# Kernel optimization log

Hardware: AMD Instinct MI355X
Metric: run time of the kernel (lower is better)

## Reference

```python
import jax, jax.numpy as jnp
import numpy as np


def _hausdorff(x, y):
    # x, y: [B, C, N, D] point sets per (batch, channel); rows are points.
    x2 = jnp.sum(x * x, axis=-1)                       # [B, C, N]
    y2 = jnp.sum(y * y, axis=-1)                       # [B, C, M]
    xy = jnp.einsum('bcnd,bcmd->bcnm', x, y)           # [B, C, N, M]
    d2 = x2[..., :, None] + y2[..., None, :] - 2.0 * xy
    d = jnp.sqrt(jnp.maximum(d2, 0.0))                 # Euclidean distances
    d_fwd = jnp.max(jnp.min(d, axis=-1), axis=-1)      # max_n min_m, [B, C]
    d_bwd = jnp.max(jnp.min(d, axis=-2), axis=-1)      # max_m min_n, [B, C]
    return jnp.maximum(d_fwd, d_bwd)                   # symmetric Hausdorff [B, C]


def setup_inputs() -> dict:
    key = jax.random.key(0)
    k1, k2 = jax.random.split(key)
    B, C, H, W = 8, 3, 1024, 1024
    inp = jax.random.normal(k1, (B, C, H, W), dtype=jnp.float32)
    tgt = jax.random.normal(k2, (B, C, H, W), dtype=jnp.float32)
    return {'input': inp, 'target': tgt}


def reference(input, target):
    h = _hausdorff(input, target)        # [B, C]
    # original: sum_i mean_c(h[i]) / B == mean over (B, C)
    return jnp.mean(h)
```

## Files before the change

### kernel.cpp

```cpp
#include <hip/hip_runtime.h>
#include <math.h>

constexpr int BC = 24;
constexpr int N  = 1024;
constexpr int D  = 1024;
constexpr int TILE = 128;
constexpr int BK = 32;
constexpr int SK = BK + 8;

typedef short short8 __attribute__((ext_vector_type(8)));
typedef float f32x4  __attribute__((ext_vector_type(4)));

#define FINF 3.402823466e+38f

#define GLDS16(g, l)                                                          \
    __builtin_amdgcn_global_load_lds(                                         \
        (const __attribute__((address_space(1))) void*)(g),                   \
        (__attribute__((address_space(3))) void*)(l), 16, 0, 0)

__device__ inline unsigned pk_bf16(float a, float b) {
    unsigned ua = __float_as_uint(a) + 0x8000u;
    unsigned ub = __float_as_uint(b) + 0x8000u;
    return __builtin_amdgcn_perm(ub, ua, 0x07060302);
}

__global__ __launch_bounds__(256) void prep_kernel(const float* __restrict__ X,
                                                   const float* __restrict__ Y,
                                                   unsigned short* __restrict__ Xbf,
                                                   unsigned short* __restrict__ Ybf,
                                                   float* __restrict__ xn,
                                                   float* __restrict__ yn) {
    int w = threadIdx.x >> 6, lane = threadIdx.x & 63;
    long rid = (long)blockIdx.x * 4 + w;
    bool isY = rid >= (long)BC * N;
    long row = isY ? rid - (long)BC * N : rid;
    const float* src = (isY ? Y : X) + row * D;
    unsigned short* dst = (isY ? Ybf : Xbf) + row * D;
    float s = 0.f;
    #pragma unroll
    for (int q = 0; q < 4; q++) {
        float4 v = ((const float4*)src)[lane + q * 64];
        s += v.x * v.x + v.y * v.y + v.z * v.z + v.w * v.w;
        uint2 p; p.x = pk_bf16(v.x, v.y); p.y = pk_bf16(v.z, v.w);
        ((uint2*)dst)[lane + q * 64] = p;
    }
    #pragma unroll
    for (int m = 1; m < 64; m <<= 1) s += __shfl_xor(s, m, 64);
    if (lane == 0) (isY ? yn : xn)[row] = s;
}

__global__ __launch_bounds__(256) void tile_bf16_kernel(const unsigned short* __restrict__ Xbf,
                                                        const unsigned short* __restrict__ Ybf,
                                                        const float* __restrict__ xn,
                                                        const float* __restrict__ yn,
                                                        unsigned* __restrict__ rowmin,
                                                        unsigned* __restrict__ colmin) {
    __shared__ unsigned short Xs[TILE * BK];
    __shared__ unsigned short Ys[TILE * BK];
    int bc = blockIdx.z, tn = blockIdx.y, tm = blockIdx.x;
    const unsigned short* Xb = Xbf + ((size_t)bc * N + (size_t)tn * TILE) * D;
    const unsigned short* Yb = Ybf + ((size_t)bc * N + (size_t)tm * TILE) * D;

    int t = threadIdx.x;
    int wave = t >> 6, lane = t & 63;
    int wr = wave >> 1, wc = wave & 1;
    int quad = lane >> 4, tx = lane & 15;

    int c0 = t, c1 = t + 256;
    const unsigned short* gx0 = Xb + (size_t)(c0 >> 2) * D + (c0 & 3) * 8;
    const unsigned short* gx1 = Xb + (size_t)(c1 >> 2) * D + (c1 & 3) * 8;
    const unsigned short* gy0 = Yb + (size_t)(c0 >> 2) * D + (c0 & 3) * 8;
    const unsigned short* gy1 = Yb + (size_t)(c1 >> 2) * D + (c1 & 3) * 8;

    f32x4 acc[4][4];
    #pragma unroll
    for (int i = 0; i < 4; i++)
        #pragma unroll
        for (int j = 0; j < 4; j++) acc[i][j] = (f32x4)0.f;

    for (int k0 = 0; k0 < D; k0 += BK) {
        __syncthreads();
        GLDS16(gx0 + k0, &Xs[c0 * 8]);
        GLDS16(gx1 + k0, &Xs[c1 * 8]);
        GLDS16(gy0 + k0, &Ys[c0 * 8]);
        GLDS16(gy1 + k0, &Ys[c1 * 8]);
        __syncthreads();

        short8 af[4], bg[4];
        #pragma unroll
        for (int mi = 0; mi < 4; mi++)
            af[mi] = *(const short8*)&Xs[(wr * 64 + mi * 16 + tx) * BK + quad * 8];
        #pragma unroll
        for (int mj = 0; mj < 4; mj++)
            bg[mj] = *(const short8*)&Ys[(wc * 64 + mj * 16 + tx) * BK + quad * 8];
        #pragma unroll
        for (int mi = 0; mi < 4; mi++)
            #pragma unroll
            for (int mj = 0; mj < 4; mj++)
                acc[mi][mj] = __builtin_amdgcn_mfma_f32_16x16x32_bf16(af[mi], bg[mj], acc[mi][mj], 0, 0, 0);
    }

    int rbase = bc * N + tn * TILE + wr * 64;
    int cbase = bc * N + tm * TILE + wc * 64;
    float xnr[4][4], ynr[4];
    #pragma unroll
    for (int mi = 0; mi < 4; mi++)
        #pragma unroll
        for (int r = 0; r < 4; r++) xnr[mi][r] = xn[rbase + mi * 16 + quad * 4 + r];
    #pragma unroll
    for (int mj = 0; mj < 4; mj++) ynr[mj] = yn[cbase + mj * 16 + tx];

    float rmin[4][4], cmin[4];
    #pragma unroll
    for (int mi = 0; mi < 4; mi++)
        #pragma unroll
        for (int r = 0; r < 4; r++) rmin[mi][r] = FINF;
    #pragma unroll
    for (int mj = 0; mj < 4; mj++) cmin[mj] = FINF;

    #pragma unroll
    for (int mi = 0; mi < 4; mi++)
        #pragma unroll
        for (int mj = 0; mj < 4; mj++)
            #pragma unroll
            for (int r = 0; r < 4; r++) {
                float d2 = fmaxf(xnr[mi][r] + ynr[mj] - 2.f * acc[mi][mj][r], 0.f);
                rmin[mi][r] = fminf(rmin[mi][r], d2);
                cmin[mj]    = fminf(cmin[mj], d2);
            }

    #pragma unroll
    for (int m = 1; m < 16; m <<= 1)
        #pragma unroll
        for (int mi = 0; mi < 4; mi++)
            #pragma unroll
            for (int r = 0; r < 4; r++)
                rmin[mi][r] = fminf(rmin[mi][r], __shfl_xor(rmin[mi][r], m, 64));
    if (tx == 0) {
        #pragma unroll
        for (int mi = 0; mi < 4; mi++)
            #pragma unroll
            for (int r = 0; r < 4; r++)
                atomicMin(&rowmin[rbase + mi * 16 + quad * 4 + r], __float_as_uint(rmin[mi][r]));
    }
    #pragma unroll
    for (int m = 16; m < 64; m <<= 1)
        #pragma unroll
        for (int mj = 0; mj < 4; mj++)
            cmin[mj] = fminf(cmin[mj], __shfl_xor(cmin[mj], m, 64));
    if (quad == 0) {
        #pragma unroll
        for (int mj = 0; mj < 4; mj++)
            atomicMin(&colmin[cbase + mj * 16 + tx], __float_as_uint(cmin[mj]));
    }
}

__global__ __launch_bounds__(256) void norms_kernel(const float* __restrict__ X,
                                                    const float* __restrict__ Y,
                                                    float* __restrict__ xn,
                                                    float* __restrict__ yn) {
    int w = threadIdx.x >> 6, lane = threadIdx.x & 63;
    long rid = (long)blockIdx.x * 4 + w;
    bool isY = rid >= (long)BC * N;
    long row = isY ? rid - (long)BC * N : rid;
    const float* src = (isY ? Y : X) + row * D;
    float s = 0.f;
    #pragma unroll
    for (int q = 0; q < 4; q++) {
        float4 v = ((const float4*)src)[lane + q * 64];
        s += v.x * v.x + v.y * v.y + v.z * v.z + v.w * v.w;
    }
    #pragma unroll
    for (int m = 1; m < 64; m <<= 1) s += __shfl_xor(s, m, 64);
    if (lane == 0) (isY ? yn : xn)[row] = s;
}

__global__ __launch_bounds__(256) void tile_conv_kernel(const float* __restrict__ X,
                                                        const float* __restrict__ Y,
                                                        const float* __restrict__ xn,
                                                        const float* __restrict__ yn,
                                                        unsigned* __restrict__ rowmin,
                                                        unsigned* __restrict__ colmin) {
    __shared__ unsigned short Xs[TILE * SK];
    __shared__ unsigned short Ys[TILE * SK];
    int bc = blockIdx.z, tn = blockIdx.y, tm = blockIdx.x;
    const float* Xb = X + ((size_t)bc * N + (size_t)tn * TILE) * D;
    const float* Yb = Y + ((size_t)bc * N + (size_t)tm * TILE) * D;

    int t = threadIdx.x;
    int srow = t >> 3, sq = t & 7;
    int wave = t >> 6, lane = t & 63;
    int wr = wave >> 1, wc = wave & 1;
    int quad = lane >> 4, tx = lane & 15;

    f32x4 acc[4][4];
    #pragma unroll
    for (int i = 0; i < 4; i++)
        #pragma unroll
        for (int j = 0; j < 4; j++) acc[i][j] = (f32x4)0.f;

    float4 xv[4], yv[4];
    #pragma unroll
    for (int i = 0; i < 4; i++) {
        xv[i] = *(const float4*)(Xb + (size_t)(srow + i * 32) * D + sq * 4);
        yv[i] = *(const float4*)(Yb + (size_t)(srow + i * 32) * D + sq * 4);
    }

    for (int k0 = 0; k0 < D; k0 += BK) {
        __syncthreads();
        #pragma unroll
        for (int i = 0; i < 4; i++) {
            uint2 px; px.x = pk_bf16(xv[i].x, xv[i].y); px.y = pk_bf16(xv[i].z, xv[i].w);
            *(uint2*)&Xs[(srow + i * 32) * SK + sq * 4] = px;
            uint2 py; py.x = pk_bf16(yv[i].x, yv[i].y); py.y = pk_bf16(yv[i].z, yv[i].w);
            *(uint2*)&Ys[(srow + i * 32) * SK + sq * 4] = py;
        }
        __syncthreads();
        if (k0 + BK < D) {
            #pragma unroll
            for (int i = 0; i < 4; i++) {
                xv[i] = *(const float4*)(Xb + (size_t)(srow + i * 32) * D + k0 + BK + sq * 4);
                yv[i] = *(const float4*)(Yb + (size_t)(srow + i * 32) * D + k0 + BK + sq * 4);
            }
        }
        short8 af[4], bg[4];
        #pragma unroll
        for (int mi = 0; mi < 4; mi++)
            af[mi] = *(const short8*)&Xs[(wr * 64 + mi * 16 + tx) * SK + quad * 8];
        #pragma unroll
        for (int mj = 0; mj < 4; mj++)
            bg[mj] = *(const short8*)&Ys[(wc * 64 + mj * 16 + tx) * SK + quad * 8];
        #pragma unroll
        for (int mi = 0; mi < 4; mi++)
            #pragma unroll
            for (int mj = 0; mj < 4; mj++)
                acc[mi][mj] = __builtin_amdgcn_mfma_f32_16x16x32_bf16(af[mi], bg[mj], acc[mi][mj], 0, 0, 0);
    }

    int rbase = bc * N + tn * TILE + wr * 64;
    int cbase = bc * N + tm * TILE + wc * 64;
    float xnr[4][4], ynr[4];
    #pragma unroll
    for (int mi = 0; mi < 4; mi++)
        #pragma unroll
        for (int r = 0; r < 4; r++) xnr[mi][r] = xn[rbase + mi * 16 + quad * 4 + r];
    #pragma unroll
    for (int mj = 0; mj < 4; mj++) ynr[mj] = yn[cbase + mj * 16 + tx];

    float rmin[4][4], cmin[4];
    #pragma unroll
    for (int mi = 0; mi < 4; mi++)
        #pragma unroll
        for (int r = 0; r < 4; r++) rmin[mi][r] = FINF;
    #pragma unroll
    for (int mj = 0; mj < 4; mj++) cmin[mj] = FINF;

    #pragma unroll
    for (int mi = 0; mi < 4; mi++)
        #pragma unroll
        for (int mj = 0; mj < 4; mj++)
            #pragma unroll
            for (int r = 0; r < 4; r++) {
                float d2 = fmaxf(xnr[mi][r] + ynr[mj] - 2.f * acc[mi][mj][r], 0.f);
                rmin[mi][r] = fminf(rmin[mi][r], d2);
                cmin[mj]    = fminf(cmin[mj], d2);
            }

    #pragma unroll
    for (int m = 1; m < 16; m <<= 1)
        #pragma unroll
        for (int mi = 0; mi < 4; mi++)
            #pragma unroll
            for (int r = 0; r < 4; r++)
                rmin[mi][r] = fminf(rmin[mi][r], __shfl_xor(rmin[mi][r], m, 64));
    if (tx == 0) {
        #pragma unroll
        for (int mi = 0; mi < 4; mi++)
            #pragma unroll
            for (int r = 0; r < 4; r++)
                atomicMin(&rowmin[rbase + mi * 16 + quad * 4 + r], __float_as_uint(rmin[mi][r]));
    }
    #pragma unroll
    for (int m = 16; m < 64; m <<= 1)
        #pragma unroll
        for (int mj = 0; mj < 4; mj++)
            cmin[mj] = fminf(cmin[mj], __shfl_xor(cmin[mj], m, 64));
    if (quad == 0) {
        #pragma unroll
        for (int mj = 0; mj < 4; mj++)
            atomicMin(&colmin[cbase + mj * 16 + tx], __float_as_uint(cmin[mj]));
    }
}

__global__ __launch_bounds__(256) void finalize_kernel(const unsigned* __restrict__ rowmin,
                                                       const unsigned* __restrict__ colmin,
                                                       float* __restrict__ out) {
    int bc = blockIdx.x;
    float v = 0.f;
    for (int i = threadIdx.x; i < N; i += 256) {
        v = fmaxf(v, __uint_as_float(rowmin[bc * N + i]));
        v = fmaxf(v, __uint_as_float(colmin[bc * N + i]));
    }
    #pragma unroll
    for (int m = 1; m < 64; m <<= 1) v = fmaxf(v, __shfl_xor(v, m, 64));
    __shared__ float ws[4];
    int lane = threadIdx.x & 63, w = threadIdx.x >> 6;
    if (lane == 0) ws[w] = v;
    __syncthreads();
    if (threadIdx.x == 0) {
        float m = fmaxf(fmaxf(ws[0], ws[1]), fmaxf(ws[2], ws[3]));
        atomicAdd(out, sqrtf(m) * (1.0f / (float)BC));
    }
}

extern "C" void kernel_launch(void* const* d_in, const int* in_sizes, int n_in,
                              void* d_out, int out_size, void* d_ws, size_t ws_size,
                              hipStream_t stream) {
    const float* X = (const float*)d_in[0];
    const float* Y = (const float*)d_in[1];
    float* out = (float*)d_out;

    unsigned* rowmin = (unsigned*)d_ws;
    unsigned* colmin = rowmin + BC * N;
    float* xn = (float*)(colmin + BC * N);
    float* yn = xn + BC * N;
    size_t head = (size_t)4 * BC * N * 4;
    size_t bf_bytes = (size_t)BC * N * D * 2;

    hipMemsetAsync(d_ws, 0xFF, (size_t)2 * BC * N * sizeof(unsigned), stream);
    hipMemsetAsync(d_out, 0, sizeof(float), stream);

    dim3 grid(N / TILE, N / TILE, BC);
    if (ws_size >= head + 2 * bf_bytes) {
        unsigned short* Xbf = (unsigned short*)((char*)d_ws + head);
        unsigned short* Ybf = Xbf + (size_t)BC * N * D;
        prep_kernel<<<2 * BC * N / 4, 256, 0, stream>>>(X, Y, Xbf, Ybf, xn, yn);
        tile_bf16_kernel<<<grid, 256, 0, stream>>>(Xbf, Ybf, xn, yn, rowmin, colmin);
    } else {
        norms_kernel<<<2 * BC * N / 4, 256, 0, stream>>>(X, Y, xn, yn);
        tile_conv_kernel<<<grid, 256, 0, stream>>>(X, Y, xn, yn, rowmin, colmin);
    }
    finalize_kernel<<<BC, 256, 0, stream>>>(rowmin, colmin, out);
}
```

Before: 312.1 us.

## Double K-tile depth with swizzled LDS and fuse memsets into prep

Raises the K step of the bf16 MFMA tile kernel from 32 to 64, using an XOR-swizzled LDS layout for the direct global-to-LDS loads so fragment reads avoid bank conflicts, and halving the number of barrier pairs per tile. The prep kernel now does four rows per wave with 16-byte stores, and it also initialises the min buffers and output, which removes two hipMemsetAsync calls on the main path. In exchange LDS use per block doubles, which may lower occupancy, and the swizzle index arithmetic must match between the load and read sides.

```diff
diff --git a/kernel.cpp b/kernel.cpp
--- a/kernel.cpp
+++ b/kernel.cpp
@@ -5,8 +5,8 @@
 constexpr int N  = 1024;
 constexpr int D  = 1024;
 constexpr int TILE = 128;
-constexpr int BK = 32;
-constexpr int SK = BK + 8;
+constexpr int BK = 64;
+constexpr int SKF = 40;
 
 typedef short short8 __attribute__((ext_vector_type(8)));
 typedef float f32x4  __attribute__((ext_vector_type(4)));
@@ -29,24 +29,37 @@
                                                    unsigned short* __restrict__ Xbf,
                                                    unsigned short* __restrict__ Ybf,
                                                    float* __restrict__ xn,
-                                                   float* __restrict__ yn) {
+                                                   float* __restrict__ yn,
+                                                   unsigned* __restrict__ minbuf,
+                                                   float* __restrict__ out) {
+    if (blockIdx.x < 2 * BC * N / 256) {
+        minbuf[blockIdx.x * 256 + threadIdx.x] = 0xFFFFFFFFu;
+        if (blockIdx.x == 0 && threadIdx.x == 0) *out = 0.f;
+    }
     int w = threadIdx.x >> 6, lane = threadIdx.x & 63;
-    long rid = (long)blockIdx.x * 4 + w;
-    bool isY = rid >= (long)BC * N;
-    long row = isY ? rid - (long)BC * N : rid;
-    const float* src = (isY ? Y : X) + row * D;
-    unsigned short* dst = (isY ? Ybf : Xbf) + row * D;
-    float s = 0.f;
-    #pragma unroll
-    for (int q = 0; q < 4; q++) {
-        float4 v = ((const float4*)src)[lane + q * 64];
-        s += v.x * v.x + v.y * v.y + v.z * v.z + v.w * v.w;
-        uint2 p; p.x = pk_bf16(v.x, v.y); p.y = pk_bf16(v.z, v.w);
-        ((uint2*)dst)[lane + q * 64] = p;
-    }
-    #pragma unroll
-    for (int m = 1; m < 64; m <<= 1) s += __shfl_xor(s, m, 64);
-    if (lane == 0) (isY ? yn : xn)[row] = s;
+    #pragma unroll
+    for (int it = 0; it < 4; it++) {
+        long rid = (long)blockIdx.x * 4 + w + (long)it * 12288;
+        bool isY = rid >= (long)BC * N;
+        long row = isY ? rid - (long)BC * N : rid;
+        const float* src = (isY ? Y : X) + row * D;
+        unsigned short* dst = (isY ? Ybf : Xbf) + row * D;
+        float s = 0.f;
+        #pragma unroll
+        for (int q = 0; q < 2; q++) {
+            float4 a = *(const float4*)(src + lane * 8 + q * 512);
+            float4 b = *(const float4*)(src + lane * 8 + q * 512 + 4);
+            s += a.x * a.x + a.y * a.y + a.z * a.z + a.w * a.w;
+            s += b.x * b.x + b.y * b.y + b.z * b.z + b.w * b.w;
+            uint4 pk;
+            pk.x = pk_bf16(a.x, a.y); pk.y = pk_bf16(a.z, a.w);
+            pk.z = pk_bf16(b.x, b.y); pk.w = pk_bf16(b.z, b.w);
+            ((uint4*)dst)[lane + q * 64] = pk;
+        }
+        #pragma unroll
+        for (int m = 1; m < 64; m <<= 1) s += __shfl_xor(s, m, 64);
+        if (lane == 0) (isY ? yn : xn)[row] = s;
+    }
 }
 
 __global__ __launch_bounds__(256) void tile_bf16_kernel(const unsigned short* __restrict__ Xbf,
@@ -66,38 +79,57 @@
     int wr = wave >> 1, wc = wave & 1;
     int quad = lane >> 4, tx = lane & 15;
 
-    int c0 = t, c1 = t + 256;
-    const unsigned short* gx0 = Xb + (size_t)(c0 >> 2) * D + (c0 & 3) * 8;
-    const unsigned short* gx1 = Xb + (size_t)(c1 >> 2) * D + (c1 & 3) * 8;
-    const unsigned short* gy0 = Yb + (size_t)(c0 >> 2) * D + (c0 & 3) * 8;
-    const unsigned short* gy1 = Yb + (size_t)(c1 >> 2) * D + (c1 & 3) * 8;
+    const unsigned short* gx[4];
+    const unsigned short* gy[4];
+    #pragma unroll
+    for (int i = 0; i < 4; i++) {
+        int p = t + 256 * i;
+        int row = p >> 3;
+        int kc = (p & 7) ^ ((p >> 4) & 7);
+        gx[i] = Xb + (size_t)row * D + kc * 8;
+        gy[i] = Yb + (size_t)row * D + kc * 8;
+    }
 
     f32x4 acc[4][4];
     #pragma unroll
     for (int i = 0; i < 4; i++)
         #pragma unroll
         for (int j = 0; j < 4; j++) acc[i][j] = (f32x4)0.f;
+
+    int aoff[2][4], boff[2][4];
+    #pragma unroll
+    for (int kh = 0; kh < 2; kh++) {
+        #pragma unroll
+        for (int mi = 0; mi < 4; mi++) {
+            int ra = wr * 64 + mi * 16 + tx;
+            aoff[kh][mi] = (ra * 8 + ((kh * 4 + quad) ^ ((ra >> 1) & 7))) * 8;
+            int rb = wc * 64 + mi * 16 + tx;
+            boff[kh][mi] = (rb * 8 + ((kh * 4 + quad) ^ ((rb >> 1) & 7))) * 8;
+        }
+    }
 
     for (int k0 = 0; k0 < D; k0 += BK) {
         __syncthreads();
-        GLDS16(gx0 + k0, &Xs[c0 * 8]);
-        GLDS16(gx1 + k0, &Xs[c1 * 8]);
-        GLDS16(gy0 + k0, &Ys[c0 * 8]);
-        GLDS16(gy1 + k0, &Ys[c1 * 8]);
+        #pragma unroll
+        for (int i = 0; i < 4; i++) {
+            GLDS16(gx[i] + k0, &Xs[(t + 256 * i) * 8]);
+            GLDS16(gy[i] + k0, &Ys[(t + 256 * i) * 8]);
+        }
         __syncthreads();
 
-        short8 af[4], bg[4];
-        #pragma unroll
-        for (int mi = 0; mi < 4; mi++)
-            af[mi] = *(const short8*)&Xs[(wr * 64 + mi * 16 + tx) * BK + quad * 8];
-        #pragma unroll
-        for (int mj = 0; mj < 4; mj++)
-            bg[mj] = *(const short8*)&Ys[(wc * 64 + mj * 16 + tx) * BK + quad * 8];
-        #pragma unroll
-        for (int mi = 0; mi < 4; mi++)
-            #pragma unroll
-            for (int mj = 0; mj < 4; mj++)
-                acc[mi][mj] = __builtin_amdgcn_mfma_f32_16x16x32_bf16(af[mi], bg[mj], acc[mi][mj], 0, 0, 0);
+        #pragma unroll
+        for (int kh = 0; kh < 2; kh++) {
+            short8 af[4], bg[4];
+            #pragma unroll
+            for (int mi = 0; mi < 4; mi++) af[mi] = *(const short8*)&Xs[aoff[kh][mi]];
+            #pragma unroll
+            for (int mj = 0; mj < 4; mj++) bg[mj] = *(const short8*)&Ys[boff[kh][mj]];
+            #pragma unroll
+            for (int mi = 0; mi < 4; mi++)
+                #pragma unroll
+                for (int mj = 0; mj < 4; mj++)
+                    acc[mi][mj] = __builtin_amdgcn_mfma_f32_16x16x32_bf16(af[mi], bg[mj], acc[mi][mj], 0, 0, 0);
+        }
     }
 
     int rbase = bc * N + tn * TILE + wr * 64;
@@ -181,8 +213,8 @@
                                                         const float* __restrict__ yn,
                                                         unsigned* __restrict__ rowmin,
                                                         unsigned* __restrict__ colmin) {
-    __shared__ unsigned short Xs[TILE * SK];
-    __shared__ unsigned short Ys[TILE * SK];
+    __shared__ unsigned short Xs[TILE * SKF];
+    __shared__ unsigned short Ys[TILE * SKF];
     int bc = blockIdx.z, tn = blockIdx.y, tm = blockIdx.x;
     const float* Xb = X + ((size_t)bc * N + (size_t)tn * TILE) * D;
     const float* Yb = Y + ((size_t)bc * N + (size_t)tm * TILE) * D;
@@ -206,30 +238,30 @@
         yv[i] = *(const float4*)(Yb + (size_t)(srow + i * 32) * D + sq * 4);
     }
 
-    for (int k0 = 0; k0 < D; k0 += BK) {
+    for (int k0 = 0; k0 < D; k0 += 32) {
         __syncthreads();
         #pragma unroll
         for (int i = 0; i < 4; i++) {
             uint2 px; px.x = pk_bf16(xv[i].x, xv[i].y); px.y = pk_bf16(xv[i].z, xv[i].w);
-            *(uint2*)&Xs[(srow + i * 32) * SK + sq * 4] = px;
+            *(uint2*)&Xs[(srow + i * 32) * SKF + sq * 4] = px;
             uint2 py; py.x = pk_bf16(yv[i].x, yv[i].y); py.y = pk_bf16(yv[i].z, yv[i].w);
-            *(uint2*)&Ys[(srow + i * 32) * SK + sq * 4] = py;
+            *(uint2*)&Ys[(srow + i * 32) * SKF + sq * 4] = py;
         }
         __syncthreads();
-        if (k0 + BK < D) {
+        if (k0 + 32 < D) {
             #pragma unroll
             for (int i = 0; i < 4; i++) {
-                xv[i] = *(const float4*)(Xb + (size_t)(srow + i * 32) * D + k0 + BK + sq * 4);
-                yv[i] = *(const float4*)(Yb + (size_t)(srow + i * 32) * D + k0 + BK + sq * 4);
+                xv[i] = *(const float4*)(Xb + (size_t)(srow + i * 32) * D + k0 + 32 + sq * 4);
+                yv[i] = *(const float4*)(Yb + (size_t)(srow + i * 32) * D + k0 + 32 + sq * 4);
             }
         }
         short8 af[4], bg[4];
         #pragma unroll
         for (int mi = 0; mi < 4; mi++)
-            af[mi] = *(const short8*)&Xs[(wr * 64 + mi * 16 + tx) * SK + quad * 8];
-        #pragma unroll
-        for (int mj = 0; mj < 4; mj++)
-            bg[mj] = *(const short8*)&Ys[(wc * 64 + mj * 16 + tx) * SK + quad * 8];
+            af[mi] = *(const short8*)&Xs[(wr * 64 + mi * 16 + tx) * SKF + quad * 8];
+        #pragma unroll
+        for (int mj = 0; mj < 4; mj++)
+            bg[mj] = *(const short8*)&Ys[(wc * 64 + mj * 16 + tx) * SKF + quad * 8];
         #pragma unroll
         for (int mi = 0; mi < 4; mi++)
             #pragma unroll
@@ -327,16 +359,15 @@
     size_t head = (size_t)4 * BC * N * 4;
     size_t bf_bytes = (size_t)BC * N * D * 2;
 
-    hipMemsetAsync(d_ws, 0xFF, (size_t)2 * BC * N * sizeof(unsigned), stream);
-    hipMemsetAsync(d_out, 0, sizeof(float), stream);
-
     dim3 grid(N / TILE, N / TILE, BC);
     if (ws_size >= head + 2 * bf_bytes) {
         unsigned short* Xbf = (unsigned short*)((char*)d_ws + head);
         unsigned short* Ybf = Xbf + (size_t)BC * N * D;
-        prep_kernel<<<2 * BC * N / 4, 256, 0, stream>>>(X, Y, Xbf, Ybf, xn, yn);
+        prep_kernel<<<3072, 256, 0, stream>>>(X, Y, Xbf, Ybf, xn, yn, rowmin, out);
         tile_bf16_kernel<<<grid, 256, 0, stream>>>(Xbf, Ybf, xn, yn, rowmin, colmin);
     } else {
+        hipMemsetAsync(d_ws, 0xFF, (size_t)2 * BC * N * sizeof(unsigned), stream);
+        hipMemsetAsync(d_out, 0, sizeof(float), stream);
         norms_kernel<<<2 * BC * N / 4, 256, 0, stream>>>(X, Y, xn, yn);
         tile_conv_kernel<<<grid, 256, 0, stream>>>(X, Y, xn, yn, rowmin, colmin);
     }
```

Result: faster. 299.7 us (-4.0%).
